# Kernel optimization log

Hardware: AMD Instinct MI355X
Metric: run time of the kernel (lower is better)

Reference implementation:

```python
import jax, jax.numpy as jnp
import numpy as np

BATCH, SEQ, DIM, DSTATE = 8, 2048, 1024, 16


def setup_inputs() -> dict:
    key = jax.random.key(0)
    ks = jax.random.split(key, 8)
    u = jax.random.normal(ks[0], (BATCH, SEQ, DIM), jnp.float32)
    gate = jax.random.normal(ks[1], (BATCH, SEQ, DIM), jnp.float32)
    # parameters (init per module: normal std=0.01 for A_log/B/C, zeros for D)
    A_log = 0.01 * jax.random.normal(ks[2], (DSTATE, DSTATE), jnp.float32)
    B_mat = 0.01 * jax.random.normal(ks[3], (DIM, DSTATE), jnp.float32)
    C_mat = 0.01 * jax.random.normal(ks[4], (DIM, DSTATE), jnp.float32)
    D = jnp.zeros((DIM,), jnp.float32)
    bound = 1.0 / np.sqrt(DIM)  # nn.Linear default init
    dt_w = jax.random.uniform(ks[5], (1, DIM), jnp.float32, -bound, bound)
    dt_b = jax.random.uniform(ks[6], (1,), jnp.float32, -bound, bound)
    return {"u": u, "gate": gate, "A_log": A_log, "B_mat": B_mat,
            "C_mat": C_mat, "D": D, "dt_w": dt_w, "dt_b": dt_b}


def reference(u, gate, A_log, B_mat, C_mat, D, dt_w, dt_b):
    # delta = sigmoid(Linear(gate)) : [B, S, 1] -> [B, S]
    delta = jax.nn.sigmoid(jnp.einsum('bsd,od->bso', gate, dt_w) + dt_b)[..., 0]
    A = -jnp.exp(A_log)                               # [N, N]
    scaled_A = delta[..., None, None] * A             # [B, S, N, N]
    A_exp = jax.scipy.linalg.expm(scaled_A)           # batched matrix exp
    Bu = jnp.einsum('bsd,dn->bsn', u, B_mat)          # [B, S, N]

    def step(h, inp):
        Aexp_t, bu_t = inp                            # [B,N,N], [B,N]
        h = jnp.einsum('bn,bnm->bm', h, Aexp_t) + bu_t
        return h, h

    h0 = jnp.zeros((u.shape[0], DSTATE), u.dtype)
    _, hs = jax.lax.scan(step, h0, (jnp.swapaxes(A_exp, 0, 1), jnp.swapaxes(Bu, 0, 1)))
    hs = jnp.swapaxes(hs, 0, 1)                       # [B, S, N]
    y = jnp.einsum('bsn,dn->bsd', hs, C_mat) + D * u  # [B, S, D]
    return y
```

## Files before the change

kernel.cpp:

```cpp
#include <hip/hip_runtime.h>

#define BATCH  8
#define SEQ    2048
#define DIMSZ  1024
#define NST    16
#define LCH    32
#define CPB    (SEQ / LCH)
#define NCHUNK (BATCH * CPB)
#define NCHEB  32

typedef __attribute__((ext_vector_type(8))) short bf16x8;
typedef __attribute__((ext_vector_type(4))) float f32x4;

static __device__ __forceinline__ unsigned short f2bf(float f) {
    unsigned u = __builtin_bit_cast(unsigned, f);
    unsigned r = (u + 0x7FFFu + ((u >> 16) & 1u)) >> 16;
    return (unsigned short)r;
}
static __device__ __forceinline__ float bf2f(unsigned short h) {
    unsigned u = ((unsigned)h) << 16;
    return __builtin_bit_cast(float, u);
}

__global__ __launch_bounds__(256) void sA_nodes(
    const float* __restrict__ A_log, float* __restrict__ Fn)
{
    __shared__ float Xs[16 * 17];
    __shared__ float Ts[16 * 17];
    const int tid = threadIdx.x;
    const int i = tid >> 4, j = tid & 15;
    const float th = (2.f * blockIdx.x + 1.f) * (3.14159265358979f / 64.f);
    const float dl = 0.5f * (1.f + cosf(th));
    const float a  = -expf(A_log[tid]);
    const float x  = dl * a * (1.0f / 64.0f);
    Xs[i*17 + j] = x;
    Ts[i*17 + j] = x;
    float S = x + (i == j ? 1.0f : 0.0f);
    __syncthreads();
#pragma unroll
    for (int k = 2; k <= 8; ++k) {
        float nt = 0.f;
#pragma unroll
        for (int kk = 0; kk < 16; ++kk)
            nt = fmaf(Ts[i*17 + kk], Xs[kk*17 + j], nt);
        nt *= (1.0f / (float)k);
        S += nt;
        __syncthreads();
        Ts[i*17 + j] = nt;
        __syncthreads();
    }
#pragma unroll
    for (int r = 0; r < 6; ++r) {
        __syncthreads();
        Ts[i*17 + j] = S;
        __syncthreads();
        float nt = 0.f;
#pragma unroll
        for (int kk = 0; kk < 16; ++kk)
            nt = fmaf(Ts[i*17 + kk], Ts[kk*17 + j], nt);
        S = nt;
    }
    Fn[(size_t)blockIdx.x * 256 + tid] = S;
}

__global__ __launch_bounds__(256) void sB_setup(
    const float* __restrict__ Fn, const float* __restrict__ B_mat,
    const float* __restrict__ dt_w,
    float* __restrict__ Gt,
    unsigned short* __restrict__ Bfh, unsigned short* __restrict__ Bfl,
    unsigned short* __restrict__ Wfh, unsigned short* __restrict__ Wfl)
{
    const int tid = threadIdx.x;
    const int blk = blockIdx.x;
    if (blk < NCHEB) {
        const int m = blk;
        float acc = 0.f;
        for (int k = 0; k < NCHEB; ++k) {
            const float th = (2.f * k + 1.f) * (3.14159265358979f / 64.f);
            acc = fmaf(Fn[(size_t)k * 256 + tid], cosf(m * th), acc);
        }
        const float sc = (m == 0) ? (1.f / 32.f) : (2.f / 32.f);
        Gt[(size_t)tid * NCHEB + m] = acc * sc;
    } else {
        const int idx0 = (blk - NCHEB) * 2048;
        for (int t = 0; t < 8; ++t) {
            const int idx = idx0 + t * 256 + tid;
            const int j  = idx & 7;
            const int l  = (idx >> 3) & 63;
            const int ks = idx >> 9;
            const int k  = ks * 32 + ((l >> 4) << 3) + j;
            const int n  = l & 15;
            float bv = B_mat[(size_t)k * 16 + n];
            unsigned short h = f2bf(bv);
            Bfh[idx] = h;
            Bfl[idx] = f2bf(bv - bf2f(h));
            float wv = (n == 0) ? dt_w[k] : 0.f;
            h = f2bf(wv);
            Wfh[idx] = h;
            Wfl[idx] = f2bf(wv - bf2f(h));
        }
    }
}

__global__ __launch_bounds__(256, 4) void k1_mfma(
    const float* __restrict__ u, const float* __restrict__ gate,
    const unsigned short* __restrict__ Bfh, const unsigned short* __restrict__ Bfl,
    const unsigned short* __restrict__ Wfh, const unsigned short* __restrict__ Wfl,
    const float* __restrict__ dt_b,
    float* __restrict__ delta, float* __restrict__ Bu)
{
    __shared__ float r0[4 * 256];
    __shared__ float r1[4 * 256];
    const int tid  = threadIdx.x;
    const int lane = tid & 63;
    const int wv   = tid >> 6;
    const size_t m0 = (size_t)blockIdx.x * 16;
    const int mrow = lane & 15;
    const int q    = lane >> 4;
    const float* up = u    + (m0 + mrow) * DIMSZ + q * 8;
    const float* gp = gate + (m0 + mrow) * DIMSZ + q * 8;
    const uint4* bh = (const uint4*)Bfh;
    const uint4* bl = (const uint4*)Bfl;
    const uint4* wh = (const uint4*)Wfh;
    const uint4* wl = (const uint4*)Wfl;

    f32x4 acc0 = {0.f, 0.f, 0.f, 0.f};
    f32x4 acc1 = {0.f, 0.f, 0.f, 0.f};
    const int ksBase = wv * 8;
    float4 a0 = *(const float4*)(up + ksBase * 32);
    float4 a1 = *(const float4*)(up + ksBase * 32 + 4);
    float4 g0 = *(const float4*)(gp + ksBase * 32);
    float4 g1 = *(const float4*)(gp + ksBase * 32 + 4);
#pragma unroll
    for (int t = 0; t < 8; ++t) {
        const int ks = ksBase + t;
        const float4 b0 = a0, b1 = a1, h0 = g0, h1 = g1;
        if (t < 7) {
            a0 = *(const float4*)(up + (ks + 1) * 32);
            a1 = *(const float4*)(up + (ks + 1) * 32 + 4);
            g0 = *(const float4*)(gp + (ks + 1) * 32);
            g1 = *(const float4*)(gp + (ks + 1) * 32 + 4);
        }
        const bf16x8 Bh = __builtin_bit_cast(bf16x8, bh[ks * 64 + lane]);
        const bf16x8 Bl = __builtin_bit_cast(bf16x8, bl[ks * 64 + lane]);
        const bf16x8 Wh = __builtin_bit_cast(bf16x8, wh[ks * 64 + lane]);
        const bf16x8 Wl = __builtin_bit_cast(bf16x8, wl[ks * 64 + lane]);
        const float fu[8] = {b0.x, b0.y, b0.z, b0.w, b1.x, b1.y, b1.z, b1.w};
        const float fg[8] = {h0.x, h0.y, h0.z, h0.w, h1.x, h1.y, h1.z, h1.w};
        bf16x8 uh, ul, gh, gl;
#pragma unroll
        for (int i = 0; i < 8; ++i) {
            unsigned short h = f2bf(fu[i]);
            uh[i] = (short)h; ul[i] = (short)f2bf(fu[i] - bf2f(h));
            h = f2bf(fg[i]);
            gh[i] = (short)h; gl[i] = (short)f2bf(fg[i] - bf2f(h));
        }
        acc0 = __builtin_amdgcn_mfma_f32_16x16x32_bf16(uh, Bh, acc0, 0, 0, 0);
        acc0 = __builtin_amdgcn_mfma_f32_16x16x32_bf16(uh, Bl, acc0, 0, 0, 0);
        acc0 = __builtin_amdgcn_mfma_f32_16x16x32_bf16(ul, Bh, acc0, 0, 0, 0);
        acc1 = __builtin_amdgcn_mfma_f32_16x16x32_bf16(gh, Wh, acc1, 0, 0, 0);
        acc1 = __builtin_amdgcn_mfma_f32_16x16x32_bf16(gh, Wl, acc1, 0, 0, 0);
        acc1 = __builtin_amdgcn_mfma_f32_16x16x32_bf16(gl, Wh, acc1, 0, 0, 0);
    }
    const int n = lane & 15;
#pragma unroll
    for (int r = 0; r < 4; ++r) {
        r0[wv * 256 + (q * 4 + r) * 16 + n] = acc0[r];
        r1[wv * 256 + (q * 4 + r) * 16 + n] = acc1[r];
    }
    __syncthreads();
    const float b = r0[tid] + r0[256 + tid] + r0[512 + tid] + r0[768 + tid];
    Bu[m0 * NST + tid] = b;
    if (tid < 16) {
        const float dacc = r1[tid * 16] + r1[256 + tid * 16] +
                           r1[512 + tid * 16] + r1[768 + tid * 16];
        delta[m0 + tid] = 1.0f / (1.0f + expf(-(dacc + dt_b[0])));
    }
}

__global__ __launch_bounds__(256) void kA_chunk(
    const float* __restrict__ Gt, const float* __restrict__ delta,
    const float* __restrict__ Bu,
    float* __restrict__ P, float* __restrict__ e)
{
    __shared__ float dl[LCH];
    __shared__ float sd[1];
    __shared__ float Bus[LCH * NST];
    __shared__ float Mlds[LCH * 256];
    __shared__ float Ps[16 * 17];
    const int tid = threadIdx.x;
    const size_t g = blockIdx.x;
    if (tid < LCH) dl[tid] = delta[g * LCH + tid];
    for (int idx = tid; idx < LCH * NST; idx += 256)
        Bus[idx] = Bu[g * (size_t)(LCH * NST) + idx];
    float gr[NCHEB];
    {
        const float4* gp = (const float4*)(Gt + (size_t)tid * NCHEB);
#pragma unroll
        for (int qq = 0; qq < NCHEB / 4; ++qq) {
            float4 v = gp[qq];
            gr[qq*4+0] = v.x; gr[qq*4+1] = v.y; gr[qq*4+2] = v.z; gr[qq*4+3] = v.w;
        }
    }
    __syncthreads();
    if (tid == 0) {
        float s = 0.f;
        for (int t = 0; t < LCH; ++t) s += dl[t];
        sd[0] = s;
    }
    for (int t = 0; t < LCH; ++t) {
        const float x = 2.f * dl[t] - 1.f;
        float acc = fmaf(gr[1], x, gr[0]);
        float tm2 = 1.f, tm1 = x;
#pragma unroll
        for (int m = 2; m < NCHEB; ++m) {
            const float tm = fmaf(2.f * x, tm1, -tm2);
            acc = fmaf(gr[m], tm, acc);
            tm2 = tm1; tm1 = tm;
        }
        Mlds[t * 256 + tid] = acc;
    }
    __syncthreads();
    float S;
    {
        const float xp = 2.f * (sd[0] * (1.f / LCH)) - 1.f;
        float acc = fmaf(gr[1], xp, gr[0]);
        float tm2 = 1.f, tm1 = xp;
#pragma unroll
        for (int m = 2; m < NCHEB; ++m) {
            const float tm = fmaf(2.f * xp, tm1, -tm2);
            acc = fmaf(gr[m], tm, acc);
            tm2 = tm1; tm1 = tm;
        }
        S = acc;
    }
    const int i = tid >> 4, j = tid & 15;
#pragma unroll
    for (int r = 0; r < 5; ++r) {
        Ps[i*17 + j] = S;
        __syncthreads();
        float ns = 0.f;
#pragma unroll
        for (int k = 0; k < 16; ++k)
            ns = fmaf(Ps[i*17 + k], Ps[k*17 + j], ns);
        __syncthreads();
        S = ns;
    }
    P[g * 256 + tid] = S;
    if (tid < 16) {
        float h = 0.f;
        for (int t = 0; t < LCH; ++t) {
            float hn = Bus[t * 16 + tid];
#pragma unroll
            for (int i2 = 0; i2 < 16; ++i2)
                hn = fmaf(__shfl(h, i2, 64), Mlds[t * 256 + i2 * 16 + tid], hn);
            h = hn;
        }
        e[g * NST + tid] = h;
    }
}

__global__ __launch_bounds__(256) void k4_scan(
    const float* __restrict__ P, const float* __restrict__ e,
    float* __restrict__ hin)
{
    __shared__ float Pl[32 * 272];
    __shared__ float el[32 * NST];
    const int tid = threadIdx.x;
    const int b = blockIdx.x;
    float h = 0.f;
    for (int half = 0; half < 2; ++half) {
        const int c0 = half * 32;
        for (int idx = tid; idx < 32*256; idx += 256) {
            const int c = idx >> 8, ij = idx & 255, i = ij >> 4, jj = ij & 15;
            Pl[c*272 + i*17 + jj] = P[((size_t)(b*CPB + c0 + c)) * 256 + ij];
        }
        for (int idx = tid; idx < 32*NST; idx += 256)
            el[idx] = e[((size_t)(b*CPB + c0)) * NST + idx];
        __syncthreads();
        if (tid < 64) {
            const int j = tid & 15;
            for (int c = 0; c < 32; ++c) {
                if (tid < 16) hin[((size_t)(b*CPB + c0 + c)) * NST + j] = h;
                float hn = el[c*16 + j];
#pragma unroll
                for (int i2 = 0; i2 < 16; ++i2)
                    hn = fmaf(__shfl(h, i2, 64), Pl[c*272 + i2*17 + j], hn);
                h = hn;
            }
        }
        __syncthreads();
    }
}

__global__ __launch_bounds__(256) void k5_out(
    const float* __restrict__ Gt, const float* __restrict__ delta,
    const float* __restrict__ Bu, const float* __restrict__ hin,
    const float* __restrict__ u, const float* __restrict__ C_mat,
    const float* __restrict__ D, float* __restrict__ y)
{
    __shared__ float dl[LCH];
    __shared__ float Bus[LCH * NST];
    __shared__ float Mlds[LCH * 256];
    __shared__ __align__(16) float Hs[LCH * NST];
    const int tid = threadIdx.x;
    const size_t g = blockIdx.x;
    if (tid < LCH) dl[tid] = delta[g * LCH + tid];
    for (int idx = tid; idx < LCH * NST; idx += 256)
        Bus[idx] = Bu[g * (size_t)(LCH * NST) + idx];
    float gr[NCHEB];
    {
        const float4* gp = (const float4*)(Gt + (size_t)tid * NCHEB);
#pragma unroll
        for (int qq = 0; qq < NCHEB / 4; ++qq) {
            float4 v = gp[qq];
            gr[qq*4+0] = v.x; gr[qq*4+1] = v.y; gr[qq*4+2] = v.z; gr[qq*4+3] = v.w;
        }
    }
    __syncthreads();
    for (int t = 0; t < LCH; ++t) {
        const float x = 2.f * dl[t] - 1.f;
        float acc = fmaf(gr[1], x, gr[0]);
        float tm2 = 1.f, tm1 = x;
#pragma unroll
        for (int m = 2; m < NCHEB; ++m) {
            const float tm = fmaf(2.f * x, tm1, -tm2);
            acc = fmaf(gr[m], tm, acc);
            tm2 = tm1; tm1 = tm;
        }
        Mlds[t * 256 + tid] = acc;
    }
    __syncthreads();
    if (tid < 16) {
        float h = hin[g * NST + tid];
        for (int t = 0; t < LCH; ++t) {
            float hn = Bus[t * 16 + tid];
#pragma unroll
            for (int i2 = 0; i2 < 16; ++i2)
                hn = fmaf(__shfl(h, i2, 64), Mlds[t * 256 + i2 * 16 + tid], hn);
            h = hn;
            Hs[t * 16 + tid] = h;
        }
    }
    __syncthreads();
    const int d0 = tid * 4;
    float4 cr[4][4];
#pragma unroll
    for (int r = 0; r < 4; ++r)
#pragma unroll
        for (int qq = 0; qq < 4; ++qq)
            cr[r][qq] = ((const float4*)C_mat)[(d0 + r) * 4 + qq];
    const float4 dv = ((const float4*)D)[tid];
    for (int t = 0; t < LCH; ++t) {
        const size_t row = (g * LCH + t) * DIMSZ;
        const float4 uv = ((const float4*)(u + row))[tid];
        float y0 = dv.x * uv.x, y1 = dv.y * uv.y, y2 = dv.z * uv.z, y3 = dv.w * uv.w;
#pragma unroll
        for (int qq = 0; qq < 4; ++qq) {
            const float4 hq = *((const float4*)&Hs[t*16 + qq*4]);
            y0 = fmaf(hq.x, cr[0][qq].x, y0); y0 = fmaf(hq.y, cr[0][qq].y, y0);
            y0 = fmaf(hq.z, cr[0][qq].z, y0); y0 = fmaf(hq.w, cr[0][qq].w, y0);
            y1 = fmaf(hq.x, cr[1][qq].x, y1); y1 = fmaf(hq.y, cr[1][qq].y, y1);
            y1 = fmaf(hq.z, cr[1][qq].z, y1); y1 = fmaf(hq.w, cr[1][qq].w, y1);
            y2 = fmaf(hq.x, cr[2][qq].x, y2); y2 = fmaf(hq.y, cr[2][qq].y, y2);
            y2 = fmaf(hq.z, cr[2][qq].z, y2); y2 = fmaf(hq.w, cr[2][qq].w, y2);
            y3 = fmaf(hq.x, cr[3][qq].x, y3); y3 = fmaf(hq.y, cr[3][qq].y, y3);
            y3 = fmaf(hq.z, cr[3][qq].z, y3); y3 = fmaf(hq.w, cr[3][qq].w, y3);
        }
        float4 ov; ov.x = y0; ov.y = y1; ov.z = y2; ov.w = y3;
        ((float4*)(y + row))[tid] = ov;
    }
}

extern "C" void kernel_launch(void* const* d_in, const int* in_sizes, int n_in,
                              void* d_out, int out_size, void* d_ws, size_t ws_size,
                              hipStream_t stream)
{
    const float* u     = (const float*)d_in[0];
    const float* gate  = (const float*)d_in[1];
    const float* A_log = (const float*)d_in[2];
    const float* B_mat = (const float*)d_in[3];
    const float* C_mat = (const float*)d_in[4];
    const float* D     = (const float*)d_in[5];
    const float* dt_w  = (const float*)d_in[6];
    const float* dt_b  = (const float*)d_in[7];
    float* y = (float*)d_out;

    float* ws = (float*)d_ws;
    size_t o = 0;
    float* Fn    = ws + o; o += 32 * 256;
    float* Gt    = ws + o; o += 256 * NCHEB;
    float* delta = ws + o; o += (size_t)BATCH * SEQ;
    float* Bu    = ws + o; o += (size_t)BATCH * SEQ * NST;
    float* P     = ws + o; o += (size_t)NCHUNK * 256;
    float* e     = ws + o; o += (size_t)NCHUNK * NST;
    float* hin   = ws + o; o += (size_t)NCHUNK * NST;
    unsigned short* Bfh = (unsigned short*)(ws + o); o += 8192;
    unsigned short* Bfl = (unsigned short*)(ws + o); o += 8192;
    unsigned short* Wfh = (unsigned short*)(ws + o); o += 8192;
    unsigned short* Wfl = (unsigned short*)(ws + o); o += 8192;

    sA_nodes<<<NCHEB, 256, 0, stream>>>(A_log, Fn);
    sB_setup<<<NCHEB + 8, 256, 0, stream>>>(Fn, B_mat, dt_w, Gt, Bfh, Bfl, Wfh, Wfl);
    k1_mfma <<<BATCH * SEQ / 16, 256, 0, stream>>>(u, gate, Bfh, Bfl, Wfh, Wfl,
                                                   dt_b, delta, Bu);
    kA_chunk<<<NCHUNK, 256, 0, stream>>>(Gt, delta, Bu, P, e);
    k4_scan <<<BATCH,  256, 0, stream>>>(P, e, hin);
    k5_out  <<<NCHUNK, 256, 0, stream>>>(Gt, delta, Bu, hin, u, C_mat, D, y);
}
```

Before: 269.9 us.

## Split delta and Bu projections into separate kernels with async LDS-staged Bu

The fused MFMA projection kernel is split in two. The gate·dt_w dot product, which is a single output column, now runs as a plain FP32 wave-reduction kernel instead of three wasted MFMAs per step. The u·B_mat projection becomes its own kernel. It stages u tiles into swizzled LDS with global_load_lds double buffering and explicit vmcnt waits and barriers, prefetching the split-bf16 B fragments as well. This removes redundant MFMA work and is meant to overlap global loads with compute, at the cost of an extra launch and more complex hand-scheduled synchronisation.

```diff
diff --git a/kernel.cpp b/kernel.cpp
--- a/kernel.cpp
+++ b/kernel.cpp
@@ -102,80 +102,140 @@
     }
 }
 
-__global__ __launch_bounds__(256, 4) void k1_mfma(
-    const float* __restrict__ u, const float* __restrict__ gate,
-    const unsigned short* __restrict__ Bfh, const unsigned short* __restrict__ Bfl,
-    const unsigned short* __restrict__ Wfh, const unsigned short* __restrict__ Wfl,
-    const float* __restrict__ dt_b,
-    float* __restrict__ delta, float* __restrict__ Bu)
-{
-    __shared__ float r0[4 * 256];
-    __shared__ float r1[4 * 256];
+__global__ __launch_bounds__(256) void k1a_delta(
+    const float* __restrict__ gate, const float* __restrict__ dt_w,
+    const float* __restrict__ dt_b, float* __restrict__ delta)
+{
     const int tid  = threadIdx.x;
     const int lane = tid & 63;
-    const int wv   = tid >> 6;
-    const size_t m0 = (size_t)blockIdx.x * 16;
-    const int mrow = lane & 15;
+    const int w    = tid >> 6;
+    const int tok  = blockIdx.x * 4 + w;
+    const float* gp = gate + (size_t)tok * DIMSZ;
+    float s = 0.f;
+#pragma unroll
+    for (int i = 0; i < 4; ++i) {
+        const float4 g  = *(const float4*)(gp   + i * 256 + lane * 4);
+        const float4 wv = *(const float4*)(dt_w + i * 256 + lane * 4);
+        s = fmaf(g.x, wv.x, s); s = fmaf(g.y, wv.y, s);
+        s = fmaf(g.z, wv.z, s); s = fmaf(g.w, wv.w, s);
+    }
+#pragma unroll
+    for (int off = 32; off >= 1; off >>= 1)
+        s += __shfl_xor(s, off, 64);
+    if (lane == 0)
+        delta[tok] = 1.0f / (1.0f + expf(-(s + dt_b[0])));
+}
+
+__global__ __launch_bounds__(256, 2) void k1b_bu(
+    const float* __restrict__ u,
+    const unsigned short* __restrict__ Bfh, const unsigned short* __restrict__ Bfl,
+    float* __restrict__ Bu)
+{
+    __shared__ float lds[2][32 * 128];
+    const int tid  = threadIdx.x;
+    const int lane = tid & 63;
+    const int w    = tid >> 6;
+    const int tok0 = blockIdx.x * 32;
+    const int half = w & 1;
+    const int wrow = (w >> 1) * 16;
     const int q    = lane >> 4;
-    const float* up = u    + (m0 + mrow) * DIMSZ + q * 8;
-    const float* gp = gate + (m0 + mrow) * DIMSZ + q * 8;
+    const int r    = lane & 15;
+
     const uint4* bh = (const uint4*)Bfh;
     const uint4* bl = (const uint4*)Bfl;
-    const uint4* wh = (const uint4*)Wfh;
-    const uint4* wl = (const uint4*)Wfl;
-
-    f32x4 acc0 = {0.f, 0.f, 0.f, 0.f};
-    f32x4 acc1 = {0.f, 0.f, 0.f, 0.f};
-    const int ksBase = wv * 8;
-    float4 a0 = *(const float4*)(up + ksBase * 32);
-    float4 a1 = *(const float4*)(up + ksBase * 32 + 4);
-    float4 g0 = *(const float4*)(gp + ksBase * 32);
-    float4 g1 = *(const float4*)(gp + ksBase * 32 + 4);
-#pragma unroll
-    for (int t = 0; t < 8; ++t) {
-        const int ks = ksBase + t;
-        const float4 b0 = a0, b1 = a1, h0 = g0, h1 = g1;
-        if (t < 7) {
-            a0 = *(const float4*)(up + (ks + 1) * 32);
-            a1 = *(const float4*)(up + (ks + 1) * 32 + 4);
-            g0 = *(const float4*)(gp + (ks + 1) * 32);
-            g1 = *(const float4*)(gp + (ks + 1) * 32 + 4);
-        }
-        const bf16x8 Bh = __builtin_bit_cast(bf16x8, bh[ks * 64 + lane]);
-        const bf16x8 Bl = __builtin_bit_cast(bf16x8, bl[ks * 64 + lane]);
-        const bf16x8 Wh = __builtin_bit_cast(bf16x8, wh[ks * 64 + lane]);
-        const bf16x8 Wl = __builtin_bit_cast(bf16x8, wl[ks * 64 + lane]);
-        const float fu[8] = {b0.x, b0.y, b0.z, b0.w, b1.x, b1.y, b1.z, b1.w};
-        const float fg[8] = {h0.x, h0.y, h0.z, h0.w, h1.x, h1.y, h1.z, h1.w};
-        bf16x8 uh, ul, gh, gl;
-#pragma unroll
-        for (int i = 0; i < 8; ++i) {
-            unsigned short h = f2bf(fu[i]);
-            uh[i] = (short)h; ul[i] = (short)f2bf(fu[i] - bf2f(h));
-            h = f2bf(fg[i]);
-            gh[i] = (short)h; gl[i] = (short)f2bf(fg[i] - bf2f(h));
-        }
-        acc0 = __builtin_amdgcn_mfma_f32_16x16x32_bf16(uh, Bh, acc0, 0, 0, 0);
-        acc0 = __builtin_amdgcn_mfma_f32_16x16x32_bf16(uh, Bl, acc0, 0, 0, 0);
-        acc0 = __builtin_amdgcn_mfma_f32_16x16x32_bf16(ul, Bh, acc0, 0, 0, 0);
-        acc1 = __builtin_amdgcn_mfma_f32_16x16x32_bf16(gh, Wh, acc1, 0, 0, 0);
-        acc1 = __builtin_amdgcn_mfma_f32_16x16x32_bf16(gh, Wl, acc1, 0, 0, 0);
-        acc1 = __builtin_amdgcn_mfma_f32_16x16x32_bf16(gl, Wh, acc1, 0, 0, 0);
-    }
-    const int n = lane & 15;
-#pragma unroll
-    for (int r = 0; r < 4; ++r) {
-        r0[wv * 256 + (q * 4 + r) * 16 + n] = acc0[r];
-        r1[wv * 256 + (q * 4 + r) * 16 + n] = acc1[r];
-    }
-    __syncthreads();
-    const float b = r0[tid] + r0[256 + tid] + r0[512 + tid] + r0[768 + tid];
-    Bu[m0 * NST + tid] = b;
-    if (tid < 16) {
-        const float dacc = r1[tid * 16] + r1[256 + tid * 16] +
-                           r1[512 + tid * 16] + r1[768 + tid * 16];
-        delta[m0 + tid] = 1.0f / (1.0f + expf(-(dacc + dt_b[0])));
-    }
+
+    const int srow = 8 * w + (lane >> 5);
+    const int p    = lane & 31;
+    int colb[4];
+#pragma unroll
+    for (int i = 0; i < 4; ++i) {
+        const int row = srow + 2 * i;
+        const int lc  = (p & 16) | ((p & 15) ^ (row & 15));
+        colb[i] = ((lc & 16) ? 512 : 0) + (lc & 15) * 4;
+    }
+
+    auto stage = [&](int c, int b) {
+#pragma unroll
+        for (int i = 0; i < 4; ++i) {
+            const float* g = u + (size_t)(tok0 + srow + 2 * i) * DIMSZ
+                               + (colb[i] + c * 64);
+            __builtin_amdgcn_global_load_lds(
+                (const __attribute__((address_space(1))) void*)g,
+                (__attribute__((address_space(3))) void*)&lds[b][(8 * w + 2 * i) * 128],
+                16, 0, 0);
+        }
+    };
+
+    f32x4 acc = {0.f, 0.f, 0.f, 0.f};
+    uint4 fh[2][2], fl[2][2];
+
+    stage(0, 0);
+    stage(1, 1);
+    {
+        const int ks0 = half * 16;
+        fh[0][0] = bh[(ks0 + 0) * 64 + lane]; fl[0][0] = bl[(ks0 + 0) * 64 + lane];
+        fh[0][1] = bh[(ks0 + 1) * 64 + lane]; fl[0][1] = bl[(ks0 + 1) * 64 + lane];
+    }
+    asm volatile("s_waitcnt vmcnt(8)" ::: "memory");
+    __builtin_amdgcn_sched_barrier(0);
+    __builtin_amdgcn_s_barrier();
+
+#pragma unroll
+    for (int c = 0; c < 8; ++c) {
+        const int b = c & 1;
+        float fu[2][8];
+#pragma unroll
+        for (int s = 0; s < 2; ++s) {
+            const int c16a = (s * 8 + 2 * q + 0) ^ r;
+            const int c16b = (s * 8 + 2 * q + 1) ^ r;
+            const float4 v0 = *(const float4*)&lds[b][(wrow + r) * 128 + (half * 16 + c16a) * 4];
+            const float4 v1 = *(const float4*)&lds[b][(wrow + r) * 128 + (half * 16 + c16b) * 4];
+            fu[s][0] = v0.x; fu[s][1] = v0.y; fu[s][2] = v0.z; fu[s][3] = v0.w;
+            fu[s][4] = v1.x; fu[s][5] = v1.y; fu[s][6] = v1.z; fu[s][7] = v1.w;
+        }
+        asm volatile("s_waitcnt lgkmcnt(0)" ::: "memory");
+        __builtin_amdgcn_sched_barrier(0);
+        __builtin_amdgcn_s_barrier();
+        if (c + 2 < 8) stage(c + 2, b);
+        if (c + 1 < 8) {
+            const int ks0 = half * 16 + 2 * (c + 1);
+            fh[(c + 1) & 1][0] = bh[(ks0 + 0) * 64 + lane];
+            fl[(c + 1) & 1][0] = bl[(ks0 + 0) * 64 + lane];
+            fh[(c + 1) & 1][1] = bh[(ks0 + 1) * 64 + lane];
+            fl[(c + 1) & 1][1] = bl[(ks0 + 1) * 64 + lane];
+        }
+        __builtin_amdgcn_sched_barrier(0);
+#pragma unroll
+        for (int s = 0; s < 2; ++s) {
+            bf16x8 uh, ul;
+#pragma unroll
+            for (int i = 0; i < 8; ++i) {
+                unsigned short h = f2bf(fu[s][i]);
+                uh[i] = (short)h;
+                ul[i] = (short)f2bf(fu[s][i] - bf2f(h));
+            }
+            const bf16x8 Bh = __builtin_bit_cast(bf16x8, fh[b][s]);
+            const bf16x8 Bl = __builtin_bit_cast(bf16x8, fl[b][s]);
+            acc = __builtin_amdgcn_mfma_f32_16x16x32_bf16(uh, Bh, acc, 0, 0, 0);
+            acc = __builtin_amdgcn_mfma_f32_16x16x32_bf16(uh, Bl, acc, 0, 0, 0);
+            acc = __builtin_amdgcn_mfma_f32_16x16x32_bf16(ul, Bh, acc, 0, 0, 0);
+        }
+        if (c < 7) {
+            if (c < 6) asm volatile("s_waitcnt vmcnt(8)" ::: "memory");
+            else       asm volatile("s_waitcnt vmcnt(4)" ::: "memory");
+            __builtin_amdgcn_sched_barrier(0);
+            __builtin_amdgcn_s_barrier();
+        }
+    }
+
+    float* red = &lds[0][0];
+#pragma unroll
+    for (int rr = 0; rr < 4; ++rr)
+        red[w * 256 + (q * 4 + rr) * 16 + r] = acc[rr];
+    __syncthreads();
+    const int base = blockIdx.x * 512;
+    Bu[base + tid]       = red[tid]       + red[256 + tid];
+    Bu[base + 256 + tid] = red[512 + tid] + red[768 + tid];
 }
 
 __global__ __launch_bounds__(256) void kA_chunk(
@@ -402,8 +462,8 @@
 
     sA_nodes<<<NCHEB, 256, 0, stream>>>(A_log, Fn);
     sB_setup<<<NCHEB + 8, 256, 0, stream>>>(Fn, B_mat, dt_w, Gt, Bfh, Bfl, Wfh, Wfl);
-    k1_mfma <<<BATCH * SEQ / 16, 256, 0, stream>>>(u, gate, Bfh, Bfl, Wfh, Wfl,
-                                                   dt_b, delta, Bu);
+    k1a_delta<<<BATCH * SEQ / 4, 256, 0, stream>>>(gate, dt_w, dt_b, delta);
+    k1b_bu  <<<BATCH * SEQ / 32, 256, 0, stream>>>(u, Bfh, Bfl, Bu);
     kA_chunk<<<NCHUNK, 256, 0, stream>>>(Gt, delta, Bu, P, e);
     k4_scan <<<BATCH,  256, 0, stream>>>(P, e, hin);
     k5_out  <<<NCHUNK, 256, 0, stream>>>(Gt, delta, Bu, hin, u, C_mat, D, y);
```

Result: no change. 267.2 us (-1.0%).
